# Optimization experiments

Measured on AMD Instinct MI355X. Metric: run time of the kernel, lower is better.

The kernel has to match this reference:

```python
import jax, jax.numpy as jnp
import numpy as np

N, E, C_IN, C_OUT = 8192, 262144, 64, 64


def setup_inputs() -> dict:
    key = jax.random.key(0)
    k1, k2, k3 = jax.random.split(key, 3)
    x = jax.random.normal(k1, (N, C_IN), dtype=jnp.float32)
    edge_index = jax.random.randint(k2, (2, E), 0, N, dtype=jnp.int32)
    # xavier_uniform init for Linear weight [out, in], zeros bias (matches reset_parameters)
    limit = float(np.sqrt(6.0 / (C_IN + C_OUT)))
    W = jax.random.uniform(k3, (C_OUT, C_IN), dtype=jnp.float32, minval=-limit, maxval=limit)
    b = jnp.zeros((C_OUT,), dtype=jnp.float32)
    return {"x": x, "edge_index": edge_index, "W": W, "b": b}


def reference(x, edge_index, W, b):
    n = x.shape[0]
    # dense adjacency with set-semantics scatter (duplicate edges collapse to 1.0)
    adj = jnp.zeros((n, n), dtype=x.dtype).at[edge_index[0], edge_index[1]].set(1.0)
    adj = adj + jnp.eye(n, dtype=x.dtype)  # diagonal can become 2.0 on self-loop edges, as in torch
    degree = adj.sum(axis=1)               # row-sum degree (asymmetric graphs use out-degree)
    dinv = jnp.where(degree > 0, degree ** -0.5, 0.0)
    norm_adj = dinv[:, None] * adj * dinv[None, :]
    h = norm_adj @ x                        # [N, C_in]
    return h @ W.T + b                      # [N, C_out]
```

## Files before the change

### kernel.cpp

```cpp
#include <hip/hip_runtime.h>

#define N_NODES 8192
#define WPR 256
#define C 64
#define CAP 512

__global__ __launch_bounds__(256) void zero_bitmap(uint4* __restrict__ bm4) {
    int i = blockIdx.x * 256 + threadIdx.x;
    bm4[i] = make_uint4(0u, 0u, 0u, 0u);
}

__global__ __launch_bounds__(256) void scatter_edges(const int* __restrict__ e, int E,
                              unsigned* __restrict__ bitmap) {
    int i = (blockIdx.x * 256 + threadIdx.x) * 2;
    if (i + 1 < E) {
        int2 rr = *(const int2*)(e + i);
        int2 cc = *(const int2*)(e + E + i);
        atomicOr(&bitmap[(size_t)rr.x * WPR + (cc.x >> 5)], 1u << (cc.x & 31));
        atomicOr(&bitmap[(size_t)rr.y * WPR + (cc.y >> 5)], 1u << (cc.y & 31));
    } else if (i < E) {
        int r = e[i], c = e[E + i];
        atomicOr(&bitmap[(size_t)r * WPR + (c >> 5)], 1u << (c & 31));
    }
}

__global__ __launch_bounds__(256) void degree_kernel(const unsigned* __restrict__ bitmap,
                               float* __restrict__ dinv) {
    int wave = threadIdx.x >> 6;
    int lane = threadIdx.x & 63;
    int r = blockIdx.x * 4 + wave;
    const uint4* row = (const uint4*)(bitmap + (size_t)r * WPR);
    uint4 v = row[lane];
    int cnt = __popc(v.x) + __popc(v.y) + __popc(v.z) + __popc(v.w);
#pragma unroll
    for (int off = 32; off; off >>= 1) cnt += __shfl_down(cnt, off);
    if (lane == 0) dinv[r] = rsqrtf((float)(cnt + 1));
}

__global__ __launch_bounds__(256) void gemm_ys(const float* __restrict__ x,
                        const float* __restrict__ W,
                        const float* __restrict__ dinv,
                        float* __restrict__ ys) {
    __shared__ float Wt[C * C];
    int tid = threadIdx.x;
    for (int i = tid; i < C * C; i += 256) {
        int o = i >> 6, k = i & 63;
        Wt[k * C + o] = W[i];
    }
    __syncthreads();
    int o = tid & 63;
    int r = blockIdx.x * 4 + (tid >> 6);
    const float* xr = x + (size_t)r * C;
    float acc = 0.0f;
#pragma unroll
    for (int k = 0; k < C; ++k) acc += xr[k] * Wt[k * C + o];
    ys[(size_t)r * C + o] = dinv[r] * acc;
}

__global__ __launch_bounds__(256) void spmm_kernel(const unsigned* __restrict__ bitmap,
                            const float* __restrict__ dinv,
                            const float* __restrict__ ys,
                            const float* __restrict__ b,
                            float* __restrict__ out) {
    __shared__ unsigned short list[4][CAP];
    int wave = threadIdx.x >> 6;
    int lane = threadIdx.x & 63;
    int r = blockIdx.x * 4 + wave;
    const uint4* row = (const uint4*)(bitmap + (size_t)r * WPR);
    uint4 v = row[lane];
    int myc = __popc(v.x) + __popc(v.y) + __popc(v.z) + __popc(v.w);

    int pre = myc;
#pragma unroll
    for (int d = 1; d < 64; d <<= 1) {
        int t = __shfl_up(pre, d);
        if (lane >= d) pre += t;
    }
    int total = __shfl(pre, 63);
    int woff = pre - myc;
    bool uselist = (total <= CAP);
    unsigned short* L = list[wave];

    if (uselist) {
        int base = lane * 128;
        unsigned bits;
        bits = v.x;
        while (bits) { L[woff++] = (unsigned short)(base       + __builtin_ctz(bits)); bits &= bits - 1; }
        bits = v.y;
        while (bits) { L[woff++] = (unsigned short)(base + 32  + __builtin_ctz(bits)); bits &= bits - 1; }
        bits = v.z;
        while (bits) { L[woff++] = (unsigned short)(base + 64  + __builtin_ctz(bits)); bits &= bits - 1; }
        bits = v.w;
        while (bits) { L[woff++] = (unsigned short)(base + 96  + __builtin_ctz(bits)); bits &= bits - 1; }
    }

    float acc = ys[(size_t)r * C + lane];
    if (uselist) {
        float a0 = 0.f, a1 = 0.f, a2 = 0.f, a3 = 0.f;
        float a4 = 0.f, a5 = 0.f, a6 = 0.f, a7 = 0.f;
        int i = 0;
        for (; i + 8 <= total; i += 8) {
            int c0 = L[i],   c1 = L[i+1], c2 = L[i+2], c3 = L[i+3];
            int c4 = L[i+4], c5 = L[i+5], c6 = L[i+6], c7 = L[i+7];
            a0 += ys[(size_t)c0 * C + lane];
            a1 += ys[(size_t)c1 * C + lane];
            a2 += ys[(size_t)c2 * C + lane];
            a3 += ys[(size_t)c3 * C + lane];
            a4 += ys[(size_t)c4 * C + lane];
            a5 += ys[(size_t)c5 * C + lane];
            a6 += ys[(size_t)c6 * C + lane];
            a7 += ys[(size_t)c7 * C + lane];
        }
        for (; i < total; ++i) acc += ys[(size_t)L[i] * C + lane];
        acc += ((a0 + a1) + (a2 + a3)) + ((a4 + a5) + (a6 + a7));
    } else {
        for (int w4i = 0; w4i < WPR / 4; ++w4i) {
            uint4 vv = row[w4i];
            int base = w4i * 128;
            unsigned bits;
            bits = vv.x; while (bits) { int c = base       + __builtin_ctz(bits); bits &= bits - 1; acc += ys[(size_t)c * C + lane]; }
            bits = vv.y; while (bits) { int c = base + 32  + __builtin_ctz(bits); bits &= bits - 1; acc += ys[(size_t)c * C + lane]; }
            bits = vv.z; while (bits) { int c = base + 64  + __builtin_ctz(bits); bits &= bits - 1; acc += ys[(size_t)c * C + lane]; }
            bits = vv.w; while (bits) { int c = base + 96  + __builtin_ctz(bits); bits &= bits - 1; acc += ys[(size_t)c * C + lane]; }
        }
    }
    out[(size_t)r * C + lane] = dinv[r] * acc + b[lane];
}

extern "C" void kernel_launch(void* const* d_in, const int* in_sizes, int n_in,
                              void* d_out, int out_size, void* d_ws, size_t ws_size,
                              hipStream_t stream) {
    const float* x  = (const float*)d_in[0];
    const int*   ei = (const int*)d_in[1];
    const float* W  = (const float*)d_in[2];
    const float* b  = (const float*)d_in[3];
    float* out = (float*)d_out;
    int E = in_sizes[1] / 2;

    unsigned* bitmap = (unsigned*)d_ws;
    float* dinv = (float*)((char*)d_ws + (size_t)N_NODES * WPR * 4);
    float* ys   = dinv + N_NODES;

    zero_bitmap<<<2048, 256, 0, stream>>>((uint4*)bitmap);
    scatter_edges<<<(E / 2 + 255) / 256, 256, 0, stream>>>(ei, E, bitmap);
    degree_kernel<<<N_NODES / 4, 256, 0, stream>>>(bitmap, dinv);
    gemm_ys<<<N_NODES / 4, 256, 0, stream>>>(x, W, dinv, ys);
    spmm_kernel<<<N_NODES / 4, 256, 0, stream>>>(bitmap, dinv, ys, b, out);
}
```

Before: 52.80 us.

## Fuse GCN pipeline into one cooperative persistent kernel with grid syncs

Replaces the five-kernel sequence (zero, scatter, degree, gemm, spmm) with a single cooperative persistent kernel that uses grid.sync between phases. The degree computation is folded into the gemm and spmm row routines, so the dinv buffer goes away. The aim is to cut kernel launch overheads and inter-kernel gaps. In exchange it adds grid-wide barrier cost, host-side occupancy and attribute queries on every call, and a scatter loop without vectorised int2 loads; a fallback multi-kernel path remains for when cooperative launch fails.

```diff
diff --git a/kernel.cpp b/kernel.cpp
--- a/kernel.cpp
+++ b/kernel.cpp
@@ -1,75 +1,38 @@
 #include <hip/hip_runtime.h>
+#include <hip/hip_cooperative_groups.h>
+
+namespace cg = cooperative_groups;
 
 #define N_NODES 8192
 #define WPR 256
 #define C 64
 #define CAP 512
-
-__global__ __launch_bounds__(256) void zero_bitmap(uint4* __restrict__ bm4) {
-    int i = blockIdx.x * 256 + threadIdx.x;
-    bm4[i] = make_uint4(0u, 0u, 0u, 0u);
-}
-
-__global__ __launch_bounds__(256) void scatter_edges(const int* __restrict__ e, int E,
-                              unsigned* __restrict__ bitmap) {
-    int i = (blockIdx.x * 256 + threadIdx.x) * 2;
-    if (i + 1 < E) {
-        int2 rr = *(const int2*)(e + i);
-        int2 cc = *(const int2*)(e + E + i);
-        atomicOr(&bitmap[(size_t)rr.x * WPR + (cc.x >> 5)], 1u << (cc.x & 31));
-        atomicOr(&bitmap[(size_t)rr.y * WPR + (cc.y >> 5)], 1u << (cc.y & 31));
-    } else if (i < E) {
-        int r = e[i], c = e[E + i];
-        atomicOr(&bitmap[(size_t)r * WPR + (c >> 5)], 1u << (c & 31));
-    }
-}
-
-__global__ __launch_bounds__(256) void degree_kernel(const unsigned* __restrict__ bitmap,
-                               float* __restrict__ dinv) {
-    int wave = threadIdx.x >> 6;
-    int lane = threadIdx.x & 63;
-    int r = blockIdx.x * 4 + wave;
+#define MAXBLK 1024
+
+
+__device__ __forceinline__ void row_deg_gemm(int r, int lane,
+        const unsigned* __restrict__ bitmap, const float* __restrict__ x,
+        const float* __restrict__ Wt, float* __restrict__ ys) {
     const uint4* row = (const uint4*)(bitmap + (size_t)r * WPR);
     uint4 v = row[lane];
     int cnt = __popc(v.x) + __popc(v.y) + __popc(v.z) + __popc(v.w);
 #pragma unroll
     for (int off = 32; off; off >>= 1) cnt += __shfl_down(cnt, off);
-    if (lane == 0) dinv[r] = rsqrtf((float)(cnt + 1));
-}
-
-__global__ __launch_bounds__(256) void gemm_ys(const float* __restrict__ x,
-                        const float* __restrict__ W,
-                        const float* __restrict__ dinv,
-                        float* __restrict__ ys) {
-    __shared__ float Wt[C * C];
-    int tid = threadIdx.x;
-    for (int i = tid; i < C * C; i += 256) {
-        int o = i >> 6, k = i & 63;
-        Wt[k * C + o] = W[i];
-    }
-    __syncthreads();
-    int o = tid & 63;
-    int r = blockIdx.x * 4 + (tid >> 6);
+    int total = __shfl(cnt, 0);
+    float dr = rsqrtf((float)(total + 1));
     const float* xr = x + (size_t)r * C;
     float acc = 0.0f;
 #pragma unroll
-    for (int k = 0; k < C; ++k) acc += xr[k] * Wt[k * C + o];
-    ys[(size_t)r * C + o] = dinv[r] * acc;
-}
-
-__global__ __launch_bounds__(256) void spmm_kernel(const unsigned* __restrict__ bitmap,
-                            const float* __restrict__ dinv,
-                            const float* __restrict__ ys,
-                            const float* __restrict__ b,
-                            float* __restrict__ out) {
-    __shared__ unsigned short list[4][CAP];
-    int wave = threadIdx.x >> 6;
-    int lane = threadIdx.x & 63;
-    int r = blockIdx.x * 4 + wave;
+    for (int k = 0; k < C; ++k) acc += xr[k] * Wt[k * C + lane];
+    ys[(size_t)r * C + lane] = dr * acc;
+}
+
+__device__ __forceinline__ void row_spmm(int r, int lane,
+        const unsigned* __restrict__ bitmap, const float* __restrict__ ys,
+        float bl, unsigned short* __restrict__ L, float* __restrict__ out) {
     const uint4* row = (const uint4*)(bitmap + (size_t)r * WPR);
     uint4 v = row[lane];
     int myc = __popc(v.x) + __popc(v.y) + __popc(v.z) + __popc(v.w);
-
     int pre = myc;
 #pragma unroll
     for (int d = 1; d < 64; d <<= 1) {
@@ -78,30 +41,20 @@
     }
     int total = __shfl(pre, 63);
     int woff = pre - myc;
-    bool uselist = (total <= CAP);
-    unsigned short* L = list[wave];
-
-    if (uselist) {
+    float dr = rsqrtf((float)(total + 1));
+    float acc = ys[(size_t)r * C + lane];
+    if (total <= CAP) {
         int base = lane * 128;
         unsigned bits;
-        bits = v.x;
-        while (bits) { L[woff++] = (unsigned short)(base       + __builtin_ctz(bits)); bits &= bits - 1; }
-        bits = v.y;
-        while (bits) { L[woff++] = (unsigned short)(base + 32  + __builtin_ctz(bits)); bits &= bits - 1; }
-        bits = v.z;
-        while (bits) { L[woff++] = (unsigned short)(base + 64  + __builtin_ctz(bits)); bits &= bits - 1; }
-        bits = v.w;
-        while (bits) { L[woff++] = (unsigned short)(base + 96  + __builtin_ctz(bits)); bits &= bits - 1; }
-    }
-
-    float acc = ys[(size_t)r * C + lane];
-    if (uselist) {
-        float a0 = 0.f, a1 = 0.f, a2 = 0.f, a3 = 0.f;
-        float a4 = 0.f, a5 = 0.f, a6 = 0.f, a7 = 0.f;
+        bits = v.x; while (bits) { L[woff++] = (unsigned short)(base       + __builtin_ctz(bits)); bits &= bits - 1; }
+        bits = v.y; while (bits) { L[woff++] = (unsigned short)(base + 32  + __builtin_ctz(bits)); bits &= bits - 1; }
+        bits = v.z; while (bits) { L[woff++] = (unsigned short)(base + 64  + __builtin_ctz(bits)); bits &= bits - 1; }
+        bits = v.w; while (bits) { L[woff++] = (unsigned short)(base + 96  + __builtin_ctz(bits)); bits &= bits - 1; }
+        float a0=0.f,a1=0.f,a2=0.f,a3=0.f,a4=0.f,a5=0.f,a6=0.f,a7=0.f;
         int i = 0;
         for (; i + 8 <= total; i += 8) {
-            int c0 = L[i],   c1 = L[i+1], c2 = L[i+2], c3 = L[i+3];
-            int c4 = L[i+4], c5 = L[i+5], c6 = L[i+6], c7 = L[i+7];
+            int c0=L[i],  c1=L[i+1],c2=L[i+2],c3=L[i+3];
+            int c4=L[i+4],c5=L[i+5],c6=L[i+6],c7=L[i+7];
             a0 += ys[(size_t)c0 * C + lane];
             a1 += ys[(size_t)c1 * C + lane];
             a2 += ys[(size_t)c2 * C + lane];
@@ -124,7 +77,91 @@
             bits = vv.w; while (bits) { int c = base + 96  + __builtin_ctz(bits); bits &= bits - 1; acc += ys[(size_t)c * C + lane]; }
         }
     }
-    out[(size_t)r * C + lane] = dinv[r] * acc + b[lane];
+    out[(size_t)r * C + lane] = dr * acc + bl;
+}
+
+__global__ __launch_bounds__(256, 4) void gcn_fused(
+    const float* __restrict__ x, const int* __restrict__ e, int E,
+    const float* __restrict__ W, const float* __restrict__ bias,
+    unsigned* __restrict__ bitmap, float* __restrict__ ys,
+    float* __restrict__ out)
+{
+    cg::grid_group grid = cg::this_grid();
+    __shared__ float Wt[C * C];
+    __shared__ unsigned short list[4][CAP];
+    const int tid = threadIdx.x, wave = tid >> 6, lane = tid & 63;
+    const int gthreads = gridDim.x * 256;
+    const int gwaves = gridDim.x * 4;
+    const int gw = blockIdx.x * 4 + wave;
+
+    {
+        uint4* bm4 = (uint4*)bitmap;
+        for (int i = blockIdx.x * 256 + tid; i < N_NODES * WPR / 4; i += gthreads)
+            bm4[i] = make_uint4(0u, 0u, 0u, 0u);
+        for (int i = tid; i < C * C; i += 256) {
+            int o = i >> 6, k = i & 63;
+            Wt[k * C + o] = W[i];
+        }
+    }
+    grid.sync();
+
+    for (int i = blockIdx.x * 256 + tid; i < E; i += gthreads) {
+        int r = e[i], c = e[E + i];
+        atomicOr(&bitmap[(size_t)r * WPR + (c >> 5)], 1u << (c & 31));
+    }
+    grid.sync();
+
+    for (int r = gw; r < N_NODES; r += gwaves)
+        row_deg_gemm(r, lane, bitmap, x, Wt, ys);
+    grid.sync();
+
+    const float bl = bias[lane];
+    for (int r = gw; r < N_NODES; r += gwaves)
+        row_spmm(r, lane, bitmap, ys, bl, list[wave], out);
+}
+
+__global__ __launch_bounds__(256) void k_zero(uint4* __restrict__ bm4) {
+    int i = blockIdx.x * 256 + threadIdx.x;
+    bm4[i] = make_uint4(0u, 0u, 0u, 0u);
+}
+
+__global__ __launch_bounds__(256) void k_scatter(const int* __restrict__ e, int E,
+                          unsigned* __restrict__ bitmap) {
+    int i = (blockIdx.x * 256 + threadIdx.x) * 2;
+    if (i + 1 < E) {
+        int2 rr = *(const int2*)(e + i);
+        int2 cc = *(const int2*)(e + E + i);
+        atomicOr(&bitmap[(size_t)rr.x * WPR + (cc.x >> 5)], 1u << (cc.x & 31));
+        atomicOr(&bitmap[(size_t)rr.y * WPR + (cc.y >> 5)], 1u << (cc.y & 31));
+    } else if (i < E) {
+        int r = e[i], c = e[E + i];
+        atomicOr(&bitmap[(size_t)r * WPR + (c >> 5)], 1u << (c & 31));
+    }
+}
+
+__global__ __launch_bounds__(256) void k_deg_gemm(const unsigned* __restrict__ bitmap,
+                           const float* __restrict__ x,
+                           const float* __restrict__ W,
+                           float* __restrict__ ys) {
+    __shared__ float Wt[C * C];
+    int tid = threadIdx.x;
+    for (int i = tid; i < C * C; i += 256) {
+        int o = i >> 6, k = i & 63;
+        Wt[k * C + o] = W[i];
+    }
+    __syncthreads();
+    int r = blockIdx.x * 4 + (tid >> 6);
+    row_deg_gemm(r, tid & 63, bitmap, x, Wt, ys);
+}
+
+__global__ __launch_bounds__(256) void k_spmm(const unsigned* __restrict__ bitmap,
+                       const float* __restrict__ ys,
+                       const float* __restrict__ bias,
+                       float* __restrict__ out) {
+    __shared__ unsigned short list[4][CAP];
+    int wave = threadIdx.x >> 6, lane = threadIdx.x & 63;
+    int r = blockIdx.x * 4 + wave;
+    row_spmm(r, lane, bitmap, ys, bias[lane], list[wave], out);
 }
 
 extern "C" void kernel_launch(void* const* d_in, const int* in_sizes, int n_in,
@@ -138,12 +175,30 @@
     int E = in_sizes[1] / 2;
 
     unsigned* bitmap = (unsigned*)d_ws;
-    float* dinv = (float*)((char*)d_ws + (size_t)N_NODES * WPR * 4);
-    float* ys   = dinv + N_NODES;
-
-    zero_bitmap<<<2048, 256, 0, stream>>>((uint4*)bitmap);
-    scatter_edges<<<(E / 2 + 255) / 256, 256, 0, stream>>>(ei, E, bitmap);
-    degree_kernel<<<N_NODES / 4, 256, 0, stream>>>(bitmap, dinv);
-    gemm_ys<<<N_NODES / 4, 256, 0, stream>>>(x, W, dinv, ys);
-    spmm_kernel<<<N_NODES / 4, 256, 0, stream>>>(bitmap, dinv, ys, b, out);
-}
+    float* ys = (float*)((char*)d_ws + (size_t)N_NODES * WPR * 4);
+
+    int dev = 0;           hipGetDevice(&dev);
+    int coop = 0;          hipDeviceGetAttribute(&coop, hipDeviceAttributeCooperativeLaunch, dev);
+    int cus = 0;           hipDeviceGetAttribute(&cus, hipDeviceAttributeMultiprocessorCount, dev);
+    int maxBlkPerCU = 0;
+    hipOccupancyMaxActiveBlocksPerMultiprocessor(&maxBlkPerCU, gcn_fused, 256, 0);
+
+    bool done = false;
+    if (coop && maxBlkPerCU > 0 && cus > 0) {
+        int grid = maxBlkPerCU * cus;
+        if (grid > MAXBLK) grid = MAXBLK;
+        if (grid >= 64) {
+            void* args[] = { (void*)&x, (void*)&ei, (void*)&E, (void*)&W,
+                             (void*)&b, (void*)&bitmap, (void*)&ys, (void*)&out };
+            hipError_t err = hipLaunchCooperativeKernel((const void*)gcn_fused,
+                                dim3(grid), dim3(256), args, 0, stream);
+            done = (err == hipSuccess);
+        }
+    }
+    if (!done) {
+        k_zero<<<N_NODES * WPR / 4 / 256, 256, 0, stream>>>((uint4*)bitmap);
+        k_scatter<<<(E / 2 + 255) / 256, 256, 0, stream>>>(ei, E, bitmap);
+        k_deg_gemm<<<N_NODES / 4, 256, 0, stream>>>(bitmap, x, W, ys);
+        k_spmm<<<N_NODES / 4, 256, 0, stream>>>(bitmap, ys, b, out);
+    }
+}
```

Result: slower. 198.2 us (+275.3%).
